# Kernel tuning notes

Hardware: AMD Instinct MI355X
Metric: run time of the kernel (lower is better)

Reference implementation:

```python
import jax, jax.numpy as jnp
import numpy as np

SHIFT = 1  # original picks +/-1 randomly; fixed to +1 for determinism


def _unfold_h3(a):
    # a: (N, C, H, W). torch.nn.functional.unfold with kernel (3,1), padding (1,0)
    # -> (N, C*3, H*W) laid out as (N, C, kh, H, W). We return (N, C, 3, H, W).
    H = a.shape[2]
    ap = jnp.pad(a, ((0, 0), (0, 0), (1, 1), (0, 0)))
    return jnp.stack([ap[:, :, k:k + H, :] for k in range(3)], axis=2)


def setup_inputs() -> dict:
    key = jax.random.key(0)
    k1, k2 = jax.random.split(key)
    x = jax.random.normal(k1, (1, 128, 14, 14), dtype=jnp.float32)
    w = jax.random.normal(k2, (256, 3, 64, 3), dtype=jnp.float32)  # self.weights[0]
    return {"x": x, "w": w}


def reference(x, w):
    # einsum 'ilkj -> iklj': (1,128,14,14) -> (1,14,128,14)
    t = jnp.transpose(x, (0, 2, 1, 3)).reshape(1, 1, 14, 1792)
    # im2col over H with kernel 3, pad 1 -> (1,1,3,14,1792), same layout as
    # torch unfold output (1, 3, 14*1792)
    t = _unfold_h3(t).reshape(1, 3, 14, 128, 14)
    # merge (14,2) -> 28, cyclic roll, split back and sum the pair
    t = t.reshape(1, 3, 28, 64, 14)
    t = jnp.roll(t, SHIFT, axis=2)
    t = t.reshape(1, 3, 14, 2, 64, 14).sum(axis=3)  # (1,3,14,64,14)
    # second cyclic roll along last spatial dim
    t = jnp.roll(t, SHIFT, axis=4)
    # second im2col over H=14 with kernel 3, pad 1
    a = t.reshape(1, 2688, 14, 1)
    a = _unfold_h3(a)  # (1,2688,3,14,1)
    t3 = a.reshape(1, 3, 14, 64, 3, 14)
    # contraction against weights (256,3,64,3) -> (1,256,14,14)
    return jnp.einsum('mjnlko,ijlk->mino', t3, w)
```

## Files before the change

### kernel.cpp

```cpp
#include <hip/hip_runtime.h>


#define WROW 580
#define TJ   68

__global__ __launch_bounds__(256) void fused_conv_kernel(
    const float* __restrict__ x,
    const float* __restrict__ w,
    float* __restrict__ out)
{
    __shared__ __align__(16) float wl[4 * WROW];
    __shared__ __align__(16) float t4l[3 * 14 * TJ];

    const int n  = blockIdx.x;
    const int i0 = blockIdx.y * 4;
    const int t  = threadIdx.x;

    const int hh = (n + 13) % 14;
    for (int p = t; p < 3 * 64 * 14; p += 256) {
        const int kh = p / (64 * 14);
        const int r  = p % (64 * 14);
        const int b  = r / 14;
        const int j  = r % 14;
        const int r0 = n + kh - 1;
        const int r1 = hh + kh - 1;
        float v = 0.f;
        if (r0 >= 0 && r0 < 14) v += x[b * 196 + r0 * 14 + j];
        if (r1 >= 0 && r1 < 14) v += x[(64 + b) * 196 + r1 * 14 + j];
        t4l[(kh * 14 + j) * TJ + b] = v;
    }

    for (int p = t; p < 4 * 144; p += 256) {
        const int il = p / 144;
        const int m  = p % 144;
        const float4 v = reinterpret_cast<const float4*>(w + (i0 + il) * 576)[m];
        const float vv[4] = {v.x, v.y, v.z, v.w};
        #pragma unroll
        for (int e = 0; e < 4; ++e) {
            const int q  = 4 * m + e;
            const int kh = q / 192;
            const int r  = q % 192;
            const int b  = r / 3;
            const int kj = r % 3;
            wl[il * WROW + (kh * 3 + kj) * 64 + b] = vv[e];
        }
    }
    __syncthreads();

    const int il = t >> 6;
    const int o  = (t >> 2) & 15;
    const int h  = t & 3;
    if (o >= 14) return;

    float4 acc = {0.f, 0.f, 0.f, 0.f};
    #pragma unroll
    for (int kh = 0; kh < 3; ++kh) {
        #pragma unroll
        for (int kj = 0; kj < 3; ++kj) {
            const int jp = o + kj - 1;
            if (jp < 0 || jp >= 14) continue;
            const int j = (jp == 0) ? 13 : jp - 1;
            const float4* wp = reinterpret_cast<const float4*>(&wl[il * WROW + (kh * 3 + kj) * 64]);
            const float4* tp = reinterpret_cast<const float4*>(&t4l[(kh * 14 + j) * TJ]);
            #pragma unroll
            for (int k = 0; k < 4; ++k) {
                const int b4 = h + 4 * k;
                const float4 wv = wp[b4];
                const float4 tv = tp[b4];
                acc.x += wv.x * tv.x;
                acc.y += wv.y * tv.y;
                acc.z += wv.z * tv.z;
                acc.w += wv.w * tv.w;
            }
        }
    }
    float s = acc.x + acc.y + acc.z + acc.w;
    s += __shfl_xor(s, 1);
    s += __shfl_xor(s, 2);
    if (h == 0) out[(i0 + il) * 196 + n * 14 + o] = s;
}

extern "C" void kernel_launch(void* const* d_in, const int* in_sizes, int n_in,
                              void* d_out, int out_size, void* d_ws, size_t ws_size,
                              hipStream_t stream) {
    const float* x   = (const float*)d_in[0];
    const float* w   = (const float*)d_in[1];
    float*       out = (float*)d_out;

    dim3 grid(14, 64);
    fused_conv_kernel<<<grid, 256, 0, stream>>>(x, w, out);
}
```

Before: 14.27 us.

## Precompute shifted im2col tensor in a separate kernel and load it vectorised

Moves construction of the rolled, summed im2col activation tensor out of the main kernel into a small pre-kernel that writes it to workspace once. The main kernel then reads its per-row slice with float4 loads instead of each of the 64 blocks per row redoing scattered, bounds-checked gathers from x. This adds a second kernel launch and a global round trip through workspace, which at this size may cost as much as the redundant gathers it removes.

```diff
diff --git a/kernel.cpp b/kernel.cpp
--- a/kernel.cpp
+++ b/kernel.cpp
@@ -4,8 +4,28 @@
 #define WROW 580
 #define TJ   68
 
+__global__ __launch_bounds__(256) void build_t4_kernel(
+    const float* __restrict__ x,
+    float* __restrict__ t4a)
+{
+    const int p = blockIdx.x * 256 + threadIdx.x;
+    if (p >= 14 * 3 * 64 * 14) return;
+    const int j  = p % 14;
+    int r        = p / 14;
+    const int b  = r % 64;  r /= 64;
+    const int kh = r % 3;
+    const int n  = r / 3;
+    const int hh = (n + 13) % 14;
+    const int r0 = n + kh - 1;
+    const int r1 = hh + kh - 1;
+    float v = 0.f;
+    if (r0 >= 0 && r0 < 14) v += x[b * 196 + r0 * 14 + j];
+    if (r1 >= 0 && r1 < 14) v += x[(64 + b) * 196 + r1 * 14 + j];
+    t4a[p] = v;
+}
+
 __global__ __launch_bounds__(256) void fused_conv_kernel(
-    const float* __restrict__ x,
+    const float* __restrict__ t4a,
     const float* __restrict__ w,
     float* __restrict__ out)
 {
@@ -16,18 +36,19 @@
     const int i0 = blockIdx.y * 4;
     const int t  = threadIdx.x;
 
-    const int hh = (n + 13) % 14;
-    for (int p = t; p < 3 * 64 * 14; p += 256) {
-        const int kh = p / (64 * 14);
-        const int r  = p % (64 * 14);
-        const int b  = r / 14;
-        const int j  = r % 14;
-        const int r0 = n + kh - 1;
-        const int r1 = hh + kh - 1;
-        float v = 0.f;
-        if (r0 >= 0 && r0 < 14) v += x[b * 196 + r0 * 14 + j];
-        if (r1 >= 0 && r1 < 14) v += x[(64 + b) * 196 + r1 * 14 + j];
-        t4l[(kh * 14 + j) * TJ + b] = v;
+    const float4* t4n = reinterpret_cast<const float4*>(t4a + n * 2688);
+    for (int m = t; m < 672; m += 256) {
+        const float4 v = t4n[m];
+        const float vv[4] = {v.x, v.y, v.z, v.w};
+        #pragma unroll
+        for (int e = 0; e < 4; ++e) {
+            const int q  = 4 * m + e;
+            const int j  = q % 14;
+            const int rr = q / 14;
+            const int b  = rr & 63;
+            const int kh = rr >> 6;
+            t4l[(kh * 14 + j) * TJ + b] = vv[e];
+        }
     }
 
     for (int p = t; p < 4 * 144; p += 256) {
@@ -86,7 +107,9 @@
     const float* x   = (const float*)d_in[0];
     const float* w   = (const float*)d_in[1];
     float*       out = (float*)d_out;
+    float*       t4a = (float*)d_ws;
 
+    build_t4_kernel<<<147, 256, 0, stream>>>(x, t4a);
     dim3 grid(14, 64);
-    fused_conv_kernel<<<grid, 256, 0, stream>>>(x, w, out);
+    fused_conv_kernel<<<grid, 256, 0, stream>>>(t4a, w, out);
 }
```

Result: slower. 16.51 us (+15.7%).
